# Kernel optimization log

Measured on AMD Instinct MI355X. Metric: run time of the kernel, lower is better.

The kernel has to match this reference:

```python
import jax, jax.numpy as jnp
import numpy as np

B, N, C, H, E = 16, 512, 128, 8, 131072
Nn = B * N
Dh = C // H
EPS = 1e-5


def setup_inputs() -> dict:
    key = jax.random.key(0)
    ks = jax.random.split(key, 16)
    s = C ** -0.5
    x = jax.random.normal(ks[0], (Nn, C), dtype=jnp.float32)
    edge_index = jax.random.randint(ks[1], (2, E), 0, Nn)
    batch = jnp.arange(Nn) // N  # B equal-sized graphs, sorted
    attn_bias = jax.random.normal(ks[2], (B, N, N, H), dtype=jnp.float32)
    return {
        "x": x,
        "edge_index": edge_index,
        "batch": batch,
        "attn_bias": attn_bias,
        "conv_w": jax.random.normal(ks[3], (C, C)) * s,
        "conv_b": jnp.zeros((C,)),
        "wq": jax.random.normal(ks[4], (C, C)) * s,
        "bq": jnp.zeros((C,)),
        "wk": jax.random.normal(ks[5], (C, C)) * s,
        "bk": jnp.zeros((C,)),
        "wv": jax.random.normal(ks[6], (C, C)) * s,
        "bv": jnp.zeros((C,)),
        "wo": jax.random.normal(ks[7], (C, C)) * s,
        "bo": jnp.zeros((C,)),
        "w1": jax.random.normal(ks[8], (C, 2 * C)) * s,
        "b1": jnp.zeros((2 * C,)),
        "w2": jax.random.normal(ks[9], (2 * C, C)) * (2 * C) ** -0.5,
        "b2": jnp.zeros((C,)),
        "g1": jnp.ones((C,)), "be1": jnp.zeros((C,)),
        "g2": jnp.ones((C,)), "be2": jnp.zeros((C,)),
        "g3": jnp.ones((C,)), "be3": jnp.zeros((C,)),
    }


def _bn(h, g, b):
    # BatchNorm1d over the node dimension (training-mode batch statistics)
    mu = h.mean(axis=0)
    var = h.var(axis=0)  # biased, matches torch normalization
    return g * (h - mu) * jax.lax.rsqrt(var + EPS) + b


def reference(x, edge_index, batch, attn_bias,
              conv_w, conv_b, wq, bq, wk, bk, wv, bv, wo, bo,
              w1, b1, w2, b2, g1, be1, g2, be2, g3, be3):
    n_nodes, ch = x.shape
    bsz, n_max, _, heads = attn_bias.shape
    dh = ch // heads

    # ---- GCN conv (self loops + symmetric norm) -> dropout(0) + residual + norm1
    loops = jnp.arange(n_nodes)
    src = jnp.concatenate([edge_index[0], loops])
    dst = jnp.concatenate([edge_index[1], loops])
    deg = jax.ops.segment_sum(jnp.ones_like(src, dtype=x.dtype), dst, num_segments=n_nodes)
    dinv = jax.lax.rsqrt(jnp.maximum(deg, 1.0))
    xw = x @ conv_w
    msg = xw[src] * (dinv[src] * dinv[dst])[:, None]
    hconv = jax.ops.segment_sum(msg, dst, num_segments=n_nodes) + conv_b
    h1 = _bn(hconv + x, g1, be1)

    # ---- dense batch (equal-sized sorted graphs -> pure reshape, mask all-valid)
    xd = x.reshape(bsz, n_max, ch)
    q = ((xd @ wq + bq) * (dh ** -0.5)).reshape(bsz, n_max, heads, dh)
    k = (xd @ wk + bk).reshape(bsz, n_max, heads, dh)
    v = (xd @ wv + bv).reshape(bsz, n_max, heads, dh)
    scores = jnp.einsum('bqhd,bkhd->bqkh', q, k) + attn_bias  # [B,N,N,H]
    probs = jax.nn.softmax(scores, axis=2)
    att = jnp.einsum('bqkh,bkhd->bqhd', probs, v).reshape(bsz, n_max, ch)
    att = att @ wo + bo
    h2 = _bn(att.reshape(n_nodes, ch) + x, g2, be2)

    # ---- combine branches, MLP with residual, norm3
    out = h1 + h2
    mlp = jax.nn.relu(out @ w1 + b1) @ w2 + b2
    return _bn(out + mlp, g3, be3)
```

## Files before the change

kernel.cpp:

```cpp
#include <hip/hip_runtime.h>
#include <cstddef>

#define NN 8192
#define CC 128

static __device__ inline unsigned f2bf_pack(float a, float b) {
  unsigned ua = __builtin_bit_cast(unsigned, a);
  ua += 0x7fffu + ((ua >> 16) & 1u);
  unsigned ub = __builtin_bit_cast(unsigned, b);
  ub += 0x7fffu + ((ub >> 16) & 1u);
  return (ua >> 16) | (ub & 0xffff0000u);
}
static __device__ inline float bf_lo(unsigned u) { return __builtin_bit_cast(float, u << 16); }
static __device__ inline float bf_hi(unsigned u) { return __builtin_bit_cast(float, u & 0xffff0000u); }

typedef const __attribute__((address_space(1))) void gvoid_t;
typedef __attribute__((address_space(3))) void lvoid_t;
static __device__ inline void glds16(const float* g, float* l) {
  __builtin_amdgcn_global_load_lds((gvoid_t*)g, (lvoid_t*)l, 16, 0, 0);
}


__global__ __launch_bounds__(256) void count_deg_int_k(const int* __restrict__ dst, int* degi, int E) {
  int i = blockIdx.x * 256 + threadIdx.x;
  if (i < E) atomicAdd(&degi[dst[i]], 1);
}

__global__ __launch_bounds__(256) void dinv_k(const int* __restrict__ degi, float* __restrict__ dinv, int n) {
  int i = blockIdx.x * 256 + threadIdx.x;
  if (i < n) dinv[i] = rsqrtf((float)(degi[i] + 1));
}

__global__ __launch_bounds__(256) void scan_k(const int* __restrict__ degi, int* __restrict__ rowstart,
                                              int* __restrict__ cursor) {
  __shared__ int partial[256];
  int t = threadIdx.x;
  int base = t * 32;
  int local[32];
  int s = 0;
#pragma unroll
  for (int i = 0; i < 32; ++i) { local[i] = s; s += degi[base + i]; }
  partial[t] = s;
  __syncthreads();
  for (int off = 1; off < 256; off <<= 1) {
    int v = (t >= off) ? partial[t - off] : 0;
    __syncthreads();
    partial[t] += v;
    __syncthreads();
  }
  int offset = partial[t] - s;
#pragma unroll
  for (int i = 0; i < 32; ++i) {
    rowstart[base + i] = offset + local[i];
    cursor[base + i] = offset + local[i];
  }
  if (t == 255) rowstart[NN] = offset + s;
}

__global__ __launch_bounds__(256) void bucket_k(const int* __restrict__ src, const int* __restrict__ dst,
    int* __restrict__ cursor, int* __restrict__ col, int E) {
  int e = blockIdx.x * 256 + threadIdx.x;
  if (e >= E) return;
  int d = dst[e];
  int pos = atomicAdd(&cursor[d], 1);
  col[pos] = src[e];
}

__global__ __launch_bounds__(256) void gather_k(const int* __restrict__ rowstart, const int* __restrict__ col,
    const float* __restrict__ xws, const float* __restrict__ dinv, const float* __restrict__ cb,
    const float* __restrict__ x, float* __restrict__ h1) {
  int d = blockIdx.x * 2 + (threadIdx.x >> 7);
  int c = threadIdx.x & 127;
  int j0 = rowstart[d], j1 = rowstart[d + 1];
  float dd = dinv[d];
  float sum = 0.f;
  float v = 0.f;
  if (j0 < j1) v = xws[(size_t)col[j0] * CC + c];
  for (int j = j0; j < j1; ++j) {
    float v_next = 0.f;
    if (j + 1 < j1) v_next = xws[(size_t)col[j + 1] * CC + c];
    sum += v;
    v = v_next;
  }
  int idx = d * CC + c;
  sum += xws[idx];
  h1[idx] = sum * dd + cb[c] + x[idx];
}


__global__ __launch_bounds__(256) void bn_stats_k(const float* __restrict__ X,
    float* __restrict__ sums, float* __restrict__ sumsq) {
  int t = threadIdx.x;
  int c = t & 127, rg = t >> 7;
  int r0 = blockIdx.x * 64;
  float s = 0.f, sq = 0.f;
  for (int i = 0; i < 32; ++i) {
    float v = X[(size_t)(r0 + rg + 2 * i) * CC + c];
    s += v; sq += v * v;
  }
  atomicAdd(&sums[c], s);
  atomicAdd(&sumsq[c], sq);
}

__global__ __launch_bounds__(256) void combine_k(const float* __restrict__ h1, const float* __restrict__ h2,
    const float* __restrict__ st, const float* __restrict__ g1, const float* __restrict__ be1,
    const float* __restrict__ g2, const float* __restrict__ be2, float* __restrict__ out) {
  int idx = blockIdx.x * 256 + threadIdx.x;
  int c = idx & 127;
  float mu1 = st[c] * (1.f / NN);
  float var1 = st[128 + c] * (1.f / NN) - mu1 * mu1;
  float sc1 = g1[c] * rsqrtf(var1 + 1e-5f);
  float sh1 = be1[c] - mu1 * sc1;
  float mu2 = st[256 + c] * (1.f / NN);
  float var2 = st[384 + c] * (1.f / NN) - mu2 * mu2;
  float sc2 = g2[c] * rsqrtf(var2 + 1e-5f);
  float sh2 = be2[c] - mu2 * sc2;
  out[idx] = sc1 * h1[idx] + sh1 + sc2 * h2[idx] + sh2;
}

__global__ __launch_bounds__(256) void bn_apply_k(const float* __restrict__ h, const float* __restrict__ st,
    const float* __restrict__ g3, const float* __restrict__ be3, float* __restrict__ out) {
  int idx = blockIdx.x * 256 + threadIdx.x;
  int c = idx & 127;
  float mu = st[512 + c] * (1.f / NN);
  float var = st[640 + c] * (1.f / NN) - mu * mu;
  float sc = g3[c] * rsqrtf(var + 1e-5f);
  float sh = be3[c] - mu * sc;
  out[idx] = sc * h[idx] + sh;
}

__global__ __launch_bounds__(256) void gemm_k(const float* __restrict__ A, const float* __restrict__ W,
    const float* __restrict__ bias, const float* __restrict__ resid, const float* __restrict__ dscale,
    float* __restrict__ out, int M, int N, int K, float scale, int relu) {
  __shared__ float As[64 * 132];
  __shared__ float Ws[128 * 64];
  int t = threadIdx.x;
  int ty = t >> 4, tx = t & 15;
  int row0 = blockIdx.x * 64, n0 = blockIdx.y * 64;
  float acc[4][4] = {};
  for (int kc = 0; kc < K; kc += 128) {
#pragma unroll
    for (int j = 0; j < 8; ++j) {
      int f = t + 256 * j;
      int r = f >> 5, c4 = f & 31;
      *(float4*)(As + r * 132 + c4 * 4) = *(const float4*)(A + (size_t)(row0 + r) * K + kc + c4 * 4);
    }
#pragma unroll
    for (int j = 0; j < 8; ++j) {
      int f = t + 256 * j;
      int kr = f >> 4, c4 = f & 15;
      *(float4*)(Ws + kr * 64 + c4 * 4) = *(const float4*)(W + (size_t)(kc + kr) * N + n0 + c4 * 4);
    }
    __syncthreads();
    for (int k0 = 0; k0 < 128; k0 += 4) {
      float a[4][4], b[4][4];
#pragma unroll
      for (int i = 0; i < 4; ++i) {
        float4 t4 = *(const float4*)(As + (4 * ty + i) * 132 + k0);
        a[i][0] = t4.x; a[i][1] = t4.y; a[i][2] = t4.z; a[i][3] = t4.w;
      }
#pragma unroll
      for (int kk = 0; kk < 4; ++kk) {
        float4 t4 = *(const float4*)(Ws + (k0 + kk) * 64 + 4 * tx);
        b[kk][0] = t4.x; b[kk][1] = t4.y; b[kk][2] = t4.z; b[kk][3] = t4.w;
      }
#pragma unroll
      for (int kk = 0; kk < 4; ++kk)
#pragma unroll
        for (int i = 0; i < 4; ++i)
#pragma unroll
          for (int j = 0; j < 4; ++j)
            acc[i][j] += a[i][kk] * b[kk][j];
    }
    __syncthreads();
  }
  float4 bv = make_float4(0.f, 0.f, 0.f, 0.f);
  if (bias) bv = *(const float4*)(bias + n0 + 4 * tx);
#pragma unroll
  for (int i = 0; i < 4; ++i) {
    int row = row0 + 4 * ty + i;
    float ds = dscale ? dscale[row] : 1.f;
    float4 r;
    r.x = (acc[i][0] + bv.x) * scale * ds;
    r.y = (acc[i][1] + bv.y) * scale * ds;
    r.z = (acc[i][2] + bv.z) * scale * ds;
    r.w = (acc[i][3] + bv.w) * scale * ds;
    if (relu) { r.x = fmaxf(r.x, 0.f); r.y = fmaxf(r.y, 0.f); r.z = fmaxf(r.z, 0.f); r.w = fmaxf(r.w, 0.f); }
    size_t o = (size_t)row * N + n0 + 4 * tx;
    if (resid) {
      float4 rv = *(const float4*)(resid + o);
      r.x += rv.x; r.y += rv.y; r.z += rv.z; r.w += rv.w;
    }
    *(float4*)(out + o) = r;
  }
}

__global__ __launch_bounds__(64, 2) void attn_k(const float* __restrict__ Q, const float* __restrict__ K,
    const float* __restrict__ V, const float* __restrict__ bias,
    unsigned* __restrict__ p0, unsigned* __restrict__ p1,
    unsigned* __restrict__ p2, unsigned* __restrict__ p3, float* __restrict__ lbuf) {
  __shared__ float SM[2][2048];
  const int t = threadIdx.x;
  const int orig = blockIdx.x;
  const int s = orig & 7;
  const int qtg = orig >> 3;
  const int b = qtg >> 4;
  const int qt = qtg & 15;
  const int qq = t >> 3;
  const int h = t & 7;
  const int node_t = b * 512 + qt * 32;
  const int key0 = s * 64;
  const size_t kvb = ((size_t)b * 512 + key0) * CC;
  const float* bbase = bias + ((size_t)node_t * 512 + key0) * 8;

  float4 qf[4][4];
#pragma unroll
  for (int r = 0; r < 4; ++r)
#pragma unroll
    for (int j = 0; j < 4; ++j)
      qf[r][j] = *(const float4*)(Q + (size_t)(node_t + qq + 8 * r) * CC + h * 16 + (((j + h) & 3) << 2));

  float4 acc[4][4];
  float l[4] = {0.f, 0.f, 0.f, 0.f};
#pragma unroll
  for (int r = 0; r < 4; ++r)
#pragma unroll
    for (int j = 0; j < 4; ++j) acc[r][j] = make_float4(0.f, 0.f, 0.f, 0.f);

  auto stage = [&](int ch, int bf) {
    const float* kg = K + kvb + ch * 512;
    const float* vg = V + kvb + ch * 512;
    float* ksl = &SM[bf][0];
    float* vsl = &SM[bf][512];
    float* bsl = &SM[bf][1024];
#pragma unroll
    for (int i = 0; i < 2; ++i) {
      glds16(kg + i * 256 + t * 4, ksl + i * 256);
      glds16(vg + i * 256 + t * 4, vsl + i * 256);
    }
#pragma unroll
    for (int i = 0; i < 4; ++i) {
      int q = i * 8 + (t >> 3);
      int kkp = (t >> 1) & 3;
      int hq = t & 1;
      int kks = (kkp - q) & 3;
      glds16(bbase + (size_t)q * 4096 + (size_t)(ch * 4 + kks) * 8 + hq * 4, bsl + i * 256);
    }
  };

  stage(0, 0);
  for (int ch = 0; ch < 16; ++ch) {
    int bf = ch & 1;
    if (ch + 1 < 16) stage(ch + 1, bf ^ 1);
    asm volatile("" ::: "memory");
    if (ch + 1 < 16) __builtin_amdgcn_s_waitcnt(0x0F78);
    else             __builtin_amdgcn_s_waitcnt(0x0F70);
    asm volatile("" ::: "memory");
    const float* ksl = &SM[bf][0];
    const float* vsl = &SM[bf][512];
    const float* bsl = &SM[bf][1024];
#pragma unroll
    for (int kk = 0; kk < 4; ++kk) {
      float4 kr[4], vr[4];
#pragma unroll
      for (int j = 0; j < 4; ++j) {
        int off = kk * 128 + h * 16 + (((j + h) & 3) << 2);
        kr[j] = *(const float4*)(ksl + off);
        vr[j] = *(const float4*)(vsl + off);
      }
      int brot = ((kk + qq) & 3) << 3;
#pragma unroll
      for (int r = 0; r < 4; ++r) {
        float sc = bsl[qq * 32 + r * 256 + brot + h];
#pragma unroll
        for (int j = 0; j < 4; ++j)
          sc += qf[r][j].x * kr[j].x + qf[r][j].y * kr[j].y
              + qf[r][j].z * kr[j].z + qf[r][j].w * kr[j].w;
        float p = __expf(sc);
        l[r] += p;
#pragma unroll
        for (int j = 0; j < 4; ++j) {
          acc[r][j].x += p * vr[j].x; acc[r][j].y += p * vr[j].y;
          acc[r][j].z += p * vr[j].z; acc[r][j].w += p * vr[j].w;
        }
      }
    }
  }

  unsigned* preg = (s < 4) ? ((s < 2) ? p0 : p1) : ((s < 6) ? p2 : p3);
  unsigned* pbase = preg + (size_t)(s & 1) * (NN * CC / 2);
#pragma unroll
  for (int r = 0; r < 4; ++r) {
    int node = node_t + qq + 8 * r;
    int slot = (node * 8 + h) * 8;
    unsigned u[8];
#pragma unroll
    for (int g = 0; g < 4; ++g) {
      int j = (g - h) & 3;
      u[2 * g]     = f2bf_pack(acc[r][j].x, acc[r][j].y);
      u[2 * g + 1] = f2bf_pack(acc[r][j].z, acc[r][j].w);
    }
    *(uint4*)(pbase + slot)     = make_uint4(u[0], u[1], u[2], u[3]);
    *(uint4*)(pbase + slot + 4) = make_uint4(u[4], u[5], u[6], u[7]);
    lbuf[s * 65536 + node * 8 + h] = l[r];
  }
}

__global__ __launch_bounds__(256) void attn_merge_k(const unsigned* __restrict__ p0,
    const unsigned* __restrict__ p1, const unsigned* __restrict__ p2, const unsigned* __restrict__ p3,
    const float* __restrict__ lbuf, float* __restrict__ out) {
  int i = blockIdx.x * 256 + threadIdx.x;
  float L = 0.f;
#pragma unroll
  for (int s = 0; s < 8; ++s) L += lbuf[s * 65536 + i];
  float inv = 1.f / L;
  float o[16];
#pragma unroll
  for (int d = 0; d < 16; ++d) o[d] = 0.f;
  const unsigned* regs[4] = {p0, p1, p2, p3};
#pragma unroll
  for (int s = 0; s < 8; ++s) {
    const unsigned* pb = regs[s >> 1] + (size_t)(s & 1) * (NN * CC / 2) + (size_t)i * 8;
    uint4 a = *(const uint4*)pb;
    uint4 b = *(const uint4*)(pb + 4);
    unsigned u[8] = {a.x, a.y, a.z, a.w, b.x, b.y, b.z, b.w};
#pragma unroll
    for (int j = 0; j < 8; ++j) {
      o[2*j]   += bf_lo(u[j]);
      o[2*j+1] += bf_hi(u[j]);
    }
  }
  float* po = out + (size_t)i * 16;
#pragma unroll
  for (int j = 0; j < 4; ++j)
    *(float4*)(po + 4 * j) = make_float4(o[4*j] * inv, o[4*j+1] * inv, o[4*j+2] * inv, o[4*j+3] * inv);
}


extern "C" void kernel_launch(void* const* d_in, const int* in_sizes, int n_in,
                              void* d_out, int out_size, void* d_ws, size_t ws_size,
                              hipStream_t stream) {
  const float* x      = (const float*)d_in[0];
  const int*   ei     = (const int*)d_in[1];
  const float* bias   = (const float*)d_in[3];
  const float* conv_w = (const float*)d_in[4];
  const float* conv_b = (const float*)d_in[5];
  const float* wq = (const float*)d_in[6];
  const float* bq = (const float*)d_in[7];
  const float* wk = (const float*)d_in[8];
  const float* bk = (const float*)d_in[9];
  const float* wv = (const float*)d_in[10];
  const float* bv = (const float*)d_in[11];
  const float* wo = (const float*)d_in[12];
  const float* bo = (const float*)d_in[13];
  const float* w1 = (const float*)d_in[14];
  const float* b1 = (const float*)d_in[15];
  const float* w2 = (const float*)d_in[16];
  const float* b2 = (const float*)d_in[17];
  const float* g1 = (const float*)d_in[18];
  const float* be1 = (const float*)d_in[19];
  const float* g2 = (const float*)d_in[20];
  const float* be2 = (const float*)d_in[21];
  const float* g3 = (const float*)d_in[22];
  const float* be3 = (const float*)d_in[23];
  int E = in_sizes[1] / 2;

  float* ws = (float*)d_ws;
  const size_t NC = (size_t)NN * CC;
  float* xw     = ws;
  float* h1pre  = ws + NC;
  float* qb     = ws + 2 * NC;
  float* kb     = ws + 3 * NC;
  float* vb     = ws + 4 * NC;
  float* h2pre  = ws + 5 * NC;
  float* outbuf = ws + 6 * NC;
  float* hid    = ws + 2 * NC;
  float* h3pre  = ws + 4 * NC;
  float* st     = ws + 7 * NC;
  float* dinv   = ws + 7 * NC + 768;
  int*   degi     = (int*)(ws + 7 * NC + 768 + NN);
  int*   rowstart = degi + NN;
  int*   cursor   = rowstart + NN + 1;
  int*   col      = cursor + NN;
  float* lbuf     = (float*)(col + E);

  hipMemsetAsync(degi, 0, NN * sizeof(int), stream);
  hipMemsetAsync(st, 0, 768 * sizeof(float), stream);

  count_deg_int_k<<<(E + 255) / 256, 256, 0, stream>>>(ei + E, degi, E);
  dinv_k<<<NN / 256, 256, 0, stream>>>(degi, dinv, NN);
  scan_k<<<1, 256, 0, stream>>>(degi, rowstart, cursor);
  bucket_k<<<(E + 255) / 256, 256, 0, stream>>>(ei, ei + E, cursor, col, E);
  gemm_k<<<dim3(NN / 64, 2), 256, 0, stream>>>(x, conv_w, nullptr, nullptr, dinv, xw, NN, CC, CC, 1.f, 0);
  gather_k<<<NN / 2, 256, 0, stream>>>(rowstart, col, xw, dinv, conv_b, x, h1pre);
  bn_stats_k<<<NN / 64, 256, 0, stream>>>(h1pre, st + 0, st + 128);

  gemm_k<<<dim3(NN / 64, 2), 256, 0, stream>>>(x, wq, bq, nullptr, nullptr, qb, NN, CC, CC, 0.25f, 0);
  gemm_k<<<dim3(NN / 64, 2), 256, 0, stream>>>(x, wk, bk, nullptr, nullptr, kb, NN, CC, CC, 1.f, 0);
  gemm_k<<<dim3(NN / 64, 2), 256, 0, stream>>>(x, wv, bv, nullptr, nullptr, vb, NN, CC, CC, 1.f, 0);
  attn_k<<<2048, 64, 0, stream>>>(qb, kb, vb, bias,
      (unsigned*)xw, (unsigned*)h2pre, (unsigned*)d_out, (unsigned*)outbuf, lbuf);
  attn_merge_k<<<65536 / 256, 256, 0, stream>>>((unsigned*)xw, (unsigned*)h2pre,
      (unsigned*)d_out, (unsigned*)outbuf, lbuf, vb);
  gemm_k<<<dim3(NN / 64, 2), 256, 0, stream>>>(vb, wo, bo, x, nullptr, h2pre, NN, CC, CC, 1.f, 0);
  bn_stats_k<<<NN / 64, 256, 0, stream>>>(h2pre, st + 256, st + 384);

  combine_k<<<NC / 256, 256, 0, stream>>>(h1pre, h2pre, st, g1, be1, g2, be2, outbuf);
  gemm_k<<<dim3(NN / 64, 4), 256, 0, stream>>>(outbuf, w1, b1, nullptr, nullptr, hid, NN, 2 * CC, CC, 1.f, 1);
  gemm_k<<<dim3(NN / 64, 2), 256, 0, stream>>>(hid, w2, b2, outbuf, nullptr, h3pre, NN, CC, 2 * CC, 1.f, 0);
  bn_stats_k<<<NN / 64, 256, 0, stream>>>(h3pre, st + 512, st + 640);
  bn_apply_k<<<NC / 256, 256, 0, stream>>>(h3pre, st, g3, be3, (float*)d_out);
}
```

Before: 474.6 us.

## Halve attention query tile and chunk size to raise occupancy

Each attention block now handles 16 queries instead of 32 and stages 2 keys per chunk instead of 4, so the grid doubles to 4096 blocks. Shared memory per block shrinks and the launch bound allows 4 blocks per SM, aiming for more latency hiding on the bias streaming. The cost is twice as many K/V loads across blocks, more loop iterations with smaller async copies, and narrower output stores.

```diff
diff --git a/kernel.cpp b/kernel.cpp
--- a/kernel.cpp
+++ b/kernel.cpp
@@ -195,72 +195,66 @@
   }
 }
 
-__global__ __launch_bounds__(64, 2) void attn_k(const float* __restrict__ Q, const float* __restrict__ K,
+__global__ __launch_bounds__(64, 4) void attn_k(const float* __restrict__ Q, const float* __restrict__ K,
     const float* __restrict__ V, const float* __restrict__ bias,
     unsigned* __restrict__ p0, unsigned* __restrict__ p1,
     unsigned* __restrict__ p2, unsigned* __restrict__ p3, float* __restrict__ lbuf) {
-  __shared__ float SM[2][2048];
+  __shared__ float SM[2][768];
   const int t = threadIdx.x;
   const int orig = blockIdx.x;
   const int s = orig & 7;
   const int qtg = orig >> 3;
-  const int b = qtg >> 4;
-  const int qt = qtg & 15;
+  const int b = qtg >> 5;
+  const int qt = qtg & 31;
   const int qq = t >> 3;
   const int h = t & 7;
-  const int node_t = b * 512 + qt * 32;
+  const int node_t = b * 512 + qt * 16;
   const int key0 = s * 64;
   const size_t kvb = ((size_t)b * 512 + key0) * CC;
   const float* bbase = bias + ((size_t)node_t * 512 + key0) * 8;
 
-  float4 qf[4][4];
-#pragma unroll
-  for (int r = 0; r < 4; ++r)
+  float4 qf[2][4];
+#pragma unroll
+  for (int r = 0; r < 2; ++r)
 #pragma unroll
     for (int j = 0; j < 4; ++j)
       qf[r][j] = *(const float4*)(Q + (size_t)(node_t + qq + 8 * r) * CC + h * 16 + (((j + h) & 3) << 2));
 
-  float4 acc[4][4];
-  float l[4] = {0.f, 0.f, 0.f, 0.f};
-#pragma unroll
-  for (int r = 0; r < 4; ++r)
+  float4 acc[2][4];
+  float l[2] = {0.f, 0.f};
+#pragma unroll
+  for (int r = 0; r < 2; ++r)
 #pragma unroll
     for (int j = 0; j < 4; ++j) acc[r][j] = make_float4(0.f, 0.f, 0.f, 0.f);
 
   auto stage = [&](int ch, int bf) {
-    const float* kg = K + kvb + ch * 512;
-    const float* vg = V + kvb + ch * 512;
+    const float* kg = K + kvb + ch * 256;
+    const float* vg = V + kvb + ch * 256;
     float* ksl = &SM[bf][0];
-    float* vsl = &SM[bf][512];
-    float* bsl = &SM[bf][1024];
-#pragma unroll
-    for (int i = 0; i < 2; ++i) {
-      glds16(kg + i * 256 + t * 4, ksl + i * 256);
-      glds16(vg + i * 256 + t * 4, vsl + i * 256);
-    }
-#pragma unroll
-    for (int i = 0; i < 4; ++i) {
-      int q = i * 8 + (t >> 3);
-      int kkp = (t >> 1) & 3;
-      int hq = t & 1;
-      int kks = (kkp - q) & 3;
-      glds16(bbase + (size_t)q * 4096 + (size_t)(ch * 4 + kks) * 8 + hq * 4, bsl + i * 256);
+    float* vsl = &SM[bf][256];
+    float* bsl = &SM[bf][512];
+    glds16(kg + t * 4, ksl);
+    glds16(vg + t * 4, vsl);
+    {
+      int q = t >> 2, kkp = (t >> 1) & 1, hq = t & 1;
+      int kks = (kkp - q) & 1;
+      glds16(bbase + (size_t)q * 4096 + (size_t)(ch * 2 + kks) * 8 + hq * 4, bsl);
     }
   };
 
   stage(0, 0);
-  for (int ch = 0; ch < 16; ++ch) {
+  for (int ch = 0; ch < 32; ++ch) {
     int bf = ch & 1;
-    if (ch + 1 < 16) stage(ch + 1, bf ^ 1);
+    if (ch + 1 < 32) stage(ch + 1, bf ^ 1);
     asm volatile("" ::: "memory");
-    if (ch + 1 < 16) __builtin_amdgcn_s_waitcnt(0x0F78);
+    if (ch + 1 < 32) __builtin_amdgcn_s_waitcnt(0x0F73);
     else             __builtin_amdgcn_s_waitcnt(0x0F70);
     asm volatile("" ::: "memory");
     const float* ksl = &SM[bf][0];
-    const float* vsl = &SM[bf][512];
-    const float* bsl = &SM[bf][1024];
-#pragma unroll
-    for (int kk = 0; kk < 4; ++kk) {
+    const float* vsl = &SM[bf][256];
+    const float* bsl = &SM[bf][512];
+#pragma unroll
+    for (int kk = 0; kk < 2; ++kk) {
       float4 kr[4], vr[4];
 #pragma unroll
       for (int j = 0; j < 4; ++j) {
@@ -268,10 +262,10 @@
         kr[j] = *(const float4*)(ksl + off);
         vr[j] = *(const float4*)(vsl + off);
       }
-      int brot = ((kk + qq) & 3) << 3;
-#pragma unroll
-      for (int r = 0; r < 4; ++r) {
-        float sc = bsl[qq * 32 + r * 256 + brot + h];
+#pragma unroll
+      for (int r = 0; r < 2; ++r) {
+        int q = qq + 8 * r;
+        float sc = bsl[q * 16 + (((kk + q) & 1) << 3) + h];
 #pragma unroll
         for (int j = 0; j < 4; ++j)
           sc += qf[r][j].x * kr[j].x + qf[r][j].y * kr[j].y
@@ -290,18 +284,16 @@
   unsigned* preg = (s < 4) ? ((s < 2) ? p0 : p1) : ((s < 6) ? p2 : p3);
   unsigned* pbase = preg + (size_t)(s & 1) * (NN * CC / 2);
 #pragma unroll
-  for (int r = 0; r < 4; ++r) {
+  for (int r = 0; r < 2; ++r) {
     int node = node_t + qq + 8 * r;
     int slot = (node * 8 + h) * 8;
-    unsigned u[8];
 #pragma unroll
     for (int g = 0; g < 4; ++g) {
       int j = (g - h) & 3;
-      u[2 * g]     = f2bf_pack(acc[r][j].x, acc[r][j].y);
-      u[2 * g + 1] = f2bf_pack(acc[r][j].z, acc[r][j].w);
-    }
-    *(uint4*)(pbase + slot)     = make_uint4(u[0], u[1], u[2], u[3]);
-    *(uint4*)(pbase + slot + 4) = make_uint4(u[4], u[5], u[6], u[7]);
+      unsigned u0 = f2bf_pack(acc[r][j].x, acc[r][j].y);
+      unsigned u1 = f2bf_pack(acc[r][j].z, acc[r][j].w);
+      *(uint2*)(pbase + slot + g * 2) = make_uint2(u0, u1);
+    }
     lbuf[s * 65536 + node * 8 + h] = l[r];
   }
 }
@@ -398,7 +390,7 @@
   gemm_k<<<dim3(NN / 64, 2), 256, 0, stream>>>(x, wq, bq, nullptr, nullptr, qb, NN, CC, CC, 0.25f, 0);
   gemm_k<<<dim3(NN / 64, 2), 256, 0, stream>>>(x, wk, bk, nullptr, nullptr, kb, NN, CC, CC, 1.f, 0);
   gemm_k<<<dim3(NN / 64, 2), 256, 0, stream>>>(x, wv, bv, nullptr, nullptr, vb, NN, CC, CC, 1.f, 0);
-  attn_k<<<2048, 64, 0, stream>>>(qb, kb, vb, bias,
+  attn_k<<<4096, 64, 0, stream>>>(qb, kb, vb, bias,
       (unsigned*)xw, (unsigned*)h2pre, (unsigned*)d_out, (unsigned*)outbuf, lbuf);
   attn_merge_k<<<65536 / 256, 256, 0, stream>>>((unsigned*)xw, (unsigned*)h2pre,
       (unsigned*)d_out, (unsigned*)outbuf, lbuf, vb);
```

New measurement: 450.7 us. 1.05x faster.
